# Optimization experiments

Hardware: AMD Instinct MI355X
Metric: run time of the kernel (lower is better)

The kernel has to match this reference:

```python
import jax, jax.numpy as jnp
import numpy as np

DIM = 96
HEADS = 4
HID = int(DIM * 2.66)  # 255, GDFN hidden width
B, H, W = 4, 128, 128


def _conv(x, w, b=None, groups=1):
    y = jax.lax.conv_general_dilated(x, w, (1, 1), 'SAME',
                                     dimension_numbers=('NCHW', 'OIHW', 'NCHW'),
                                     feature_group_count=groups)
    return y if b is None else y + b[None, :, None, None]


def _ln(x, w, b):
    # WithBias LayerNorm over channel dim (per pixel), biased variance, eps=1e-5
    mu = x.mean(1, keepdims=True)
    var = ((x - mu) ** 2).mean(1, keepdims=True)
    return (x - mu) / jnp.sqrt(var + 1e-5) * w[None, :, None, None] + b[None, :, None, None]


def _l2norm(x):
    # torch F.normalize(dim=-1): x / max(||x||_2, 1e-12)
    return x / jnp.maximum(jnp.linalg.norm(x, axis=-1, keepdims=True), 1e-12)


def _gelu(x):
    return jax.nn.gelu(x, approximate=False)


def setup_inputs() -> dict:
    key = jax.random.key(0)
    ks = iter(jax.random.split(key, 32))
    nrm = lambda shp, s=0.02: jax.random.normal(next(ks), shp, dtype=jnp.float32) * s
    d, h2 = DIM, HID
    inp = {
        'x': jax.random.normal(next(ks), (B, DIM, H, W), dtype=jnp.float32),
        # L_conv: 3x3(d->d,+b) GELU 1x1(d->1,+b)
        'Lc_w1': nrm((d, d, 3, 3)), 'Lc_b1': jnp.zeros((d,), jnp.float32),
        'Lc_w2': nrm((1, d, 1, 1)), 'Lc_b2': jnp.zeros((1,), jnp.float32),
        # R_conv: 3x3(d->d,+b) GELU 1x1(d->3,+b)
        'Rc_w1': nrm((d, d, 3, 3)), 'Rc_b1': jnp.zeros((d,), jnp.float32),
        'Rc_w2': nrm((3, d, 1, 1)), 'Rc_b2': jnp.zeros((3,), jnp.float32),
        # L_rein: 3x3(1->d,+b) GELU ; R_rein: 3x3(3->d,+b)
        'Lr_w': nrm((d, 1, 3, 3)), 'Lr_b': jnp.zeros((d,), jnp.float32),
        'Rr_w': nrm((d, 3, 3, 3)), 'Rr_b': jnp.zeros((d,), jnp.float32),
        # LayerNorms (WithBias)
        'n1_w': jnp.ones((d,), jnp.float32), 'n1_b': jnp.zeros((d,), jnp.float32),
        'nL_w': jnp.ones((d,), jnp.float32), 'nL_b': jnp.zeros((d,), jnp.float32),
        'n2_w': jnp.ones((d,), jnp.float32), 'n2_b': jnp.zeros((d,), jnp.float32),
        # Illum_Attention (bias=False)
        'temp': jnp.ones((HEADS, 1, 1), jnp.float32),
        'q_w': nrm((d, d, 1, 1)),
        'qd_w': nrm((d, d, 3, 3)),          # q_dwconv is a FULL 3x3 conv (no groups)
        'kv_w': nrm((2 * d, d, 1, 1)),
        'kvd_w': nrm((2 * d, 1, 3, 3)),     # depthwise, groups=2*dim
        'po_w': nrm((d, d, 1, 1)),
        # FeedForward (bias=False); NOTE: 'dwconv' here is a FULL 3x3 conv
        'pi_w': nrm((h2, d, 1, 1)),
        'fdw_w': nrm((h2, h2, 3, 3)),
        'fpo_w': nrm((d, h2, 1, 1)),
    }
    return inp


def reference(x, Lc_w1, Lc_b1, Lc_w2, Lc_b2, Rc_w1, Rc_b1, Rc_w2, Rc_b2,
              Lr_w, Lr_b, Rr_w, Rr_b, n1_w, n1_b, nL_w, nL_b, n2_w, n2_b,
              temp, q_w, qd_w, kv_w, kvd_w, po_w, pi_w, fdw_w, fpo_w):
    b, c, h, w = x.shape
    # Retinex decomposition heads
    L = _conv(_gelu(_conv(x, Lc_w1, Lc_b1)), Lc_w2, Lc_b2)   # [b,1,h,w]
    R = _conv(_gelu(_conv(x, Rc_w1, Rc_b1)), Rc_w2, Rc_b2)   # [b,3,h,w]
    L_rein = _gelu(_conv(jax.lax.stop_gradient(L), Lr_w, Lr_b))  # detach in torch
    R_rein = _conv(jax.lax.stop_gradient(R), Rr_w, Rr_b)
    # Illum_Guided_TransformerBlock: x = x + attn(norm1(x), normL(illum))
    xn = _ln(x, n1_w, n1_b)
    ill = _ln(L_rein, nL_w, nL_b)
    q = _conv(_conv(ill, q_w), qd_w)
    kv = _conv(_conv(xn, kv_w), kvd_w, groups=2 * c)
    k, v = jnp.split(kv, 2, axis=1)
    ch, hw = c // HEADS, h * w
    heads = lambda t: t.reshape(b, HEADS, ch, hw)
    qh, kh, vh = _l2norm(heads(q)), _l2norm(heads(k)), heads(v)
    # channel-wise attention: [b,heads,ch,ch]
    attn = jax.nn.softmax(jnp.einsum('bhci,bhdi->bhcd', qh, kh) * temp[None], axis=-1)
    out = jnp.einsum('bhcd,bhdi->bhci', attn, vh).reshape(b, c, h, w)
    x = x + _conv(out, po_w)
    # x = x + ffn(norm2(x))
    x2 = _ln(x, n2_w, n2_b)
    x = x + _conv(_gelu(_conv(_conv(x2, pi_w), fdw_w)), fpo_w)
    x = x + R_rein
    return (x, L, R)
```

## Files before the change

kernel.cpp:

```cpp
#include <hip/hip_runtime.h>

#define HWsz 16384
#define Wd 128

typedef unsigned short ushortT;
typedef unsigned int uintT;
typedef __attribute__((ext_vector_type(8))) short short8v;
typedef __attribute__((ext_vector_type(4))) float f32x4;
typedef __attribute__((ext_vector_type(16))) float f32x16;
typedef __attribute__((ext_vector_type(4))) unsigned short ushort4v;

__device__ __forceinline__ float gelu_f(float x){
    return 0.5f * x * (1.0f + erff(x * 0.70710678118654752f));
}
__device__ __forceinline__ ushortT f2b(float f){
    union { float f; uintT u; } v; v.f = f;
    uintT r = v.u + 0x7FFFu + ((v.u >> 16) & 1u);
    return (ushortT)(r >> 16);
}
__device__ __forceinline__ float b2f(ushortT u){
    union { uintT u; float f; } v; v.u = ((uintT)u) << 16; return v.f;
}
__device__ __forceinline__ void gload_lds16(const ushortT* g, ushortT* l){
    __builtin_amdgcn_global_load_lds(
        (const __attribute__((address_space(1))) void*)g,
        (__attribute__((address_space(3))) void*)l, 16, 0, 0);
}

__device__ __forceinline__ void pack3_one(int e, const float* __restrict__ w,
    ushortT* __restrict__ outp, int cout, int cin, int BN, int NCH)
{
    int j = e & 7; int r = e >> 3;
    int ocl = r % BN; r /= BN;
    int kg  = r & 3;  r >>= 2;
    int tap = r % 9;  r /= 9;
    int ch  = r % NCH;
    int nt  = r / NCH;
    int ci = ch*32 + kg*8 + j;
    int oc = nt*BN + ocl;
    float v = (oc < cout && ci < cin) ? w[((size_t)oc*cin + ci)*9 + tap] : 0.f;
    outp[e] = f2b(v);
}
__device__ __forceinline__ void pack1_one(int e, const float* __restrict__ w,
    ushortT* __restrict__ outp, int cout, int cin, int BN, int NCH)
{
    int j = e & 7; int r = e >> 3;
    int ocl = r % BN; r /= BN;
    int kg  = r & 3;  r >>= 2;
    int ch  = r % NCH;
    int nt  = r / NCH;
    int ci = ch*32 + kg*8 + j;
    int oc = nt*BN + ocl;
    float v = (oc < cout && ci < cin) ? w[(size_t)oc*cin + ci] : 0.f;
    outp[e] = f2b(v);
}
__global__ __launch_bounds__(256) void pack_all_kernel(
    const float* Lc, const float* Rc, const float* Qd, const float* Fd,
    const float* Q1, const float* KV1, const float* PI1, const float* FPO1,
    ushortT* dL, ushortT* dR, ushortT* dQ, ushortT* dF,
    ushortT* dq0, ushortT* dkv, ushortT* dpi, ushortT* dfpo)
{
    int e = blockIdx.x*256 + threadIdx.x;
    if      (e < 82944)  pack3_one(e,        Lc, dL, 96, 96, 48, 3);
    else if (e < 165888) pack3_one(e-82944,  Rc, dR, 96, 96, 48, 3);
    else if (e < 248832) pack3_one(e-165888, Qd, dQ, 96, 96, 32, 3);
    else if (e < 838656) pack3_one(e-248832, Fd, dF, 255,255, 64, 8);
    else if (e < 847872) pack1_one(e-838656, Q1, dq0, 96, 96, 96, 3);
    else if (e < 866304) pack1_one(e-847872, KV1,dkv, 192,96, 48, 3);
    else if (e < 890880) pack1_one(e-866304, PI1,dpi, 255,96, 64, 3);
    else if (e < 915456) pack1_one(e-890880, FPO1,dfpo,96,255, 96, 8);
}

__global__ __launch_bounds__(256) void tonhwc_kernel(
    const float* __restrict__ in, ushortT* __restrict__ outp)
{
    const int p = blockIdx.x*256 + threadIdx.x;
    const int b = blockIdx.y;
    const float* ip = in + (size_t)b*96*HWsz + p;
    ushortT* op = outp + ((size_t)b*HWsz + p)*96;
#pragma unroll
    for (int g=0; g<12; g++){
        float v[8];
#pragma unroll
        for (int c=0;c<8;c++) v[c] = ip[(size_t)(g*8+c)*HWsz];
        uint4 pk;
        pk.x = (uintT)f2b(v[0]) | ((uintT)f2b(v[1])<<16);
        pk.y = (uintT)f2b(v[2]) | ((uintT)f2b(v[3])<<16);
        pk.z = (uintT)f2b(v[4]) | ((uintT)f2b(v[5])<<16);
        pk.w = (uintT)f2b(v[6]) | ((uintT)f2b(v[7])<<16);
        *(uint4*)(op + g*8) = pk;
    }
}

template<int NG, int NCH, int ACT, int TWOOUT>
__global__ __launch_bounds__(256,2) void conv3x3_v4(
    const ushortT* __restrict__ inh,
    const ushortT* __restrict__ wpk1, const ushortT* __restrict__ wpk2,
    const float* __restrict__ bias1, const float* __restrict__ bias2,
    ushortT* __restrict__ out1, ushortT* __restrict__ out2,
    int cout, int ocpad)
{
    constexpr int BN = NG*16;
    constexpr int Cpad = NCH*32;
    constexpr int WCH4 = 9*4*BN;
    constexpr int WI = (WCH4 + 255)/256;
    __shared__ __align__(16) ushortT As[4*324*8];
    __shared__ __align__(16) ushortT Ws[WCH4*8];

    const int tid = threadIdx.x;
    const int l   = tid & 63;
    const int wv  = tid >> 6;
    const int l15 = l & 15;
    const int kg  = l >> 4;
    const int tix = blockIdx.x & 7, tiy = blockIdx.x >> 3;
    const int b   = blockIdx.z;
    const int x0 = tix*16, y0 = tiy*16;

    int nt = blockIdx.y;
    const ushortT* wpk; const float* bias; ushortT* outp; int ntw;
    if (TWOOUT && nt >= 2){ wpk = wpk2; bias = bias2; outp = out2; ntw = nt-2; }
    else { wpk = wpk1; bias = bias1; outp = out1; ntw = nt; }
    const int ocbase = ntw*BN;

    f32x4 acc[4][NG];
#pragma unroll
    for (int m=0;m<4;m++)
#pragma unroll
        for (int n=0;n<NG;n++) acc[m][n] = (f32x4){0.f,0.f,0.f,0.f};

    const ushortT* inb = inh + (size_t)b*HWsz*Cpad;

    for (int ch=0; ch<NCH; ch++){
        __syncthreads();
        for (int t=tid; t<1296; t+=256){
            int p = t>>2, g = t&3;
            int hy = p/18, hx = p - hy*18;
            int gy = y0 + hy - 1, gx = x0 + hx - 1;
            uint4 v; v.x=0u; v.y=0u; v.z=0u; v.w=0u;
            if ((unsigned)gy < 128u && (unsigned)gx < 128u)
                v = *(const uint4*)(inb + (size_t)(gy*Wd+gx)*Cpad + ch*32 + g*8);
            *(uint4*)(As + (g*324+p)*8) = v;
        }
        {
            const ushortT* wsrc = wpk + ((size_t)ntw*NCH + ch)*(WCH4*8);
#pragma unroll
            for (int i=0; i<WI; i++){
                int t = i*256 + tid;
                if ((WCH4 & 255) == 0 || t < WCH4)
                    gload_lds16(wsrc + (size_t)t*8, Ws + (size_t)t*8);
            }
        }
        __syncthreads();
#pragma unroll
        for (int tp=0; tp<9; tp++){
            const int dy = tp/3, dx = tp - dy*3;
            short8v bf[NG];
#pragma unroll
            for (int n=0;n<NG;n++)
                bf[n] = *(const short8v*)(Ws + ((size_t)(tp*4 + kg)*BN + n*16 + l15)*8);
#pragma unroll
            for (int mg=0;mg<4;mg++){
                short8v a = *(const short8v*)(As + (kg*324 + (wv*4+mg+dy)*18 + l15+dx)*8);
#pragma unroll
                for (int n=0;n<NG;n++)
                    acc[mg][n] = __builtin_amdgcn_mfma_f32_16x16x32_bf16(a, bf[n], acc[mg][n], 0,0,0);
            }
        }
    }
    __syncthreads();
    ushortT* Ts = As + wv*1024;
#pragma unroll
    for (int mg=0;mg<4;mg++){
        int gy = y0 + wv*4 + mg;
        ushortT* orow = outp + ((size_t)b*HWsz + gy*Wd + x0)*ocpad + ocbase;
#pragma unroll
        for (int n=0;n<NG;n++){
            int ocl = n*16 + l15;
            int oc  = ocbase + ocl;
            float bs = (bias && oc < cout) ? bias[oc] : 0.f;
#pragma unroll
            for (int j=0;j<4;j++){
                int pxj = kg*4 + j;
                float r = 0.f;
                if (oc < cout){ r = acc[mg][n][j] + bs; if (ACT) r = gelu_f(r); }
                int seg = ((ocl>>3) + pxj) & 7;
                Ts[pxj*64 + seg*8 + (ocl&7)] = f2b(r);
            }
        }
#pragma unroll
        for (int ps=0; ps < (BN+31)/32; ps++){
            int rpx = l & 15;
            int rs  = (l>>4) + ps*4;
            if (rs*8 < BN){
                int pseg = (rs + rpx) & 7;
                short8v v = *(const short8v*)(Ts + rpx*64 + pseg*8);
                *(short8v*)(orow + (size_t)rpx*ocpad + rs*8) = v;
            }
        }
    }
}

template<int NGW, int NCH>
__global__ __launch_bounds__(256) void gemm1x1_v2(
    const ushortT* __restrict__ inh, const ushortT* __restrict__ wpk,
    ushortT* __restrict__ outp, int cout, int ocpad)
{
    constexpr int BN = NGW*16;
    constexpr int Cpad = NCH*32;
    __shared__ __align__(16) ushortT Ts[4*16*64];

    const int tid = threadIdx.x;
    const int l = tid & 63, wv = tid >> 6, l15 = l & 15, kg = l >> 4;
    const int p0 = blockIdx.x*64;
    const int b  = blockIdx.z;
    const int nt = wv, ocbase = wv*BN;
    const ushortT* inb = inh + (size_t)b*HWsz*Cpad;

    f32x4 acc[4][NGW];
#pragma unroll
    for (int m=0;m<4;m++)
#pragma unroll
        for (int n=0;n<NGW;n++) acc[m][n] = (f32x4){0.f,0.f,0.f,0.f};

#pragma unroll
    for (int ch=0; ch<NCH; ch++){
        short8v a[4], bw[NGW];
#pragma unroll
        for (int mg=0; mg<4; mg++)
            a[mg] = *(const short8v*)(inb + (size_t)(p0 + mg*16 + l15)*Cpad + ch*32 + kg*8);
#pragma unroll
        for (int n=0;n<NGW;n++)
            bw[n] = *(const short8v*)(wpk + (((size_t)(nt*NCH + ch)*4 + kg)*BN + n*16 + l15)*8);
#pragma unroll
        for (int mg=0;mg<4;mg++)
#pragma unroll
            for (int n=0;n<NGW;n++)
                acc[mg][n] = __builtin_amdgcn_mfma_f32_16x16x32_bf16(a[mg], bw[n], acc[mg][n], 0,0,0);
    }
    ushortT* Tw = Ts + wv*1024;
#pragma unroll
    for (int mg=0;mg<4;mg++){
        ushortT* orow = outp + ((size_t)b*HWsz + p0 + mg*16)*ocpad + ocbase;
#pragma unroll
        for (int n=0;n<NGW;n++){
            int ocl = n*16 + l15;
            int oc  = ocbase + ocl;
#pragma unroll
            for (int j=0;j<4;j++){
                int pxj = kg*4 + j;
                float r = (oc < cout) ? acc[mg][n][j] : 0.f;
                int seg = ((ocl>>3) + pxj) & 7;
                Tw[pxj*64 + seg*8 + (ocl&7)] = f2b(r);
            }
        }
#pragma unroll
        for (int ps=0; ps < (BN+31)/32; ps++){
            int rpx = l & 15;
            int rs  = (l>>4) + ps*4;
            if (rs*8 < BN){
                int pseg = (rs + rpx) & 7;
                short8v v = *(const short8v*)(Tw + rpx*64 + pseg*8);
                *(short8v*)(orow + (size_t)rpx*ocpad + rs*8) = v;
            }
        }
    }
}

template<int NG, int NCH, int ACT, int OMODE, int NSPLIT, int XMAP>
__global__ __launch_bounds__(256,4) void conv3x3_mfma(
    const ushortT* __restrict__ inh,
    const ushortT* __restrict__ wpk1, const ushortT* __restrict__ wpk2,
    const float* __restrict__ bias1, const float* __restrict__ bias2,
    void* __restrict__ out1, void* __restrict__ out2,
    int cout, int ocpad)
{
    constexpr int BN = NG*16;
    constexpr int Cpad = NCH*32;
    __shared__ __align__(16) ushortT As[4*324*8];

    const int tid = threadIdx.x;
    const int l   = tid & 63;
    const int wv  = tid >> 6;
    const int l15 = l & 15;
    const int kg  = l >> 4;
    int tile = blockIdx.x, nt = blockIdx.y, b = blockIdx.z;
    const int tix = tile & 7, tiy = tile >> 3;

    const ushortT* wpk = wpk1; const float* bias = bias1; void* outv = out1;
    if (NSPLIT > 0 && nt >= NSPLIT){ nt -= NSPLIT; wpk = wpk2; bias = bias2; outv = out2; }

    f32x4 acc[4][NG];
#pragma unroll
    for (int m=0;m<4;m++)
#pragma unroll
        for (int n=0;n<NG;n++) acc[m][n] = (f32x4){0.f,0.f,0.f,0.f};

    const ushortT* inb = inh + (size_t)b*HWsz*Cpad;

    for (int ch=0; ch<NCH; ch++){
        __syncthreads();
#pragma unroll
        for (int g=0; g<4; g++){
            for (int p=tid; p<324; p+=256){
                int hy = p/18, hx = p - hy*18;
                int gy = tiy*16 + hy - 1, gx = tix*16 + hx - 1;
                uint4 v; v.x=0u; v.y=0u; v.z=0u; v.w=0u;
                if ((unsigned)gy < 128u && (unsigned)gx < 128u)
                    v = *(const uint4*)(inb + (size_t)(gy*Wd+gx)*Cpad + ch*32 + g*8);
                *(uint4*)(As + (g*324+p)*8) = v;
            }
        }
        __syncthreads();
        const ushortT* wch = wpk + (size_t)(nt*NCH + ch)*(9*4*BN*8);
#pragma unroll
        for (int tp=0; tp<9; tp++){
            const int dy = tp/3, dx = tp - dy*3;
            short8v a[4], bf[NG];
#pragma unroll
            for (int mg=0; mg<4; mg++){
                int p = (wv*4 + mg + dy)*18 + l15 + dx;
                a[mg] = *(const short8v*)(As + (kg*324 + p)*8);
            }
#pragma unroll
            for (int n=0;n<NG;n++)
                bf[n] = *(const short8v*)(wch + ((size_t)(tp*4 + kg)*BN + n*16 + l15)*8);
#pragma unroll
            for (int mg=0;mg<4;mg++)
#pragma unroll
                for (int n=0;n<NG;n++)
                    acc[mg][n] = __builtin_amdgcn_mfma_f32_16x16x32_bf16(a[mg], bf[n], acc[mg][n], 0,0,0);
        }
    }
    if (OMODE == 2){
        ushortT* out = (ushortT*)outv;
#pragma unroll
        for (int n=0;n<NG;n++){
            int oc = nt*BN + n*16 + l15;
            if (oc < cout){
                float bs = bias ? bias[oc] : 0.f;
#pragma unroll
                for (int mg=0;mg<4;mg++){
                    int gy = tiy*16 + wv*4 + mg;
                    int gx = tix*16 + kg*4;
                    ushort4v pk;
#pragma unroll
                    for (int j=0;j<4;j++){
                        float r = acc[mg][n][j] + bs;
                        if (ACT) r = gelu_f(r);
                        pk[j] = f2b(r);
                    }
                    *(ushort4v*)(out + ((size_t)b*cout + oc)*HWsz + gy*Wd + gx) = pk;
                }
            }
        }
    }
}

template<int NG, int NCH, int RES, int OMODE, int XMAP>
__global__ __launch_bounds__(256) void gemm1x1_mfma(
    const ushortT* __restrict__ inh, const ushortT* __restrict__ wpk, int wstride_z,
    const float* __restrict__ res1, const ushortT* __restrict__ res2b,
    void* __restrict__ outv, int cout, int ocpad)
{
    constexpr int BN = NG*16;
    constexpr int Cpad = NCH*32;
    constexpr int LSTR = (BN <= 64) ? 64 : 128;
    constexpr int MASK = LSTR/8 - 1;
    __shared__ __align__(16) ushortT TsS[(OMODE==1) ? 4*16*LSTR : 16];

    const int tid = threadIdx.x;
    const int l = tid & 63, wv = tid >> 6, l15 = l & 15, kg = l >> 4;
    int chunk = blockIdx.x, nt = blockIdx.y, b = blockIdx.z;
    const int p0 = chunk*256 + wv*64;
    const ushortT* inb = inh + (size_t)b*HWsz*Cpad;
    const ushortT* wp  = wpk + (size_t)b*wstride_z;

    f32x4 acc[4][NG];
#pragma unroll
    for (int m=0;m<4;m++)
#pragma unroll
        for (int n=0;n<NG;n++) acc[m][n] = (f32x4){0.f,0.f,0.f,0.f};

#pragma unroll
    for (int ch=0; ch<NCH; ch++){
        short8v a[4], bw[NG];
#pragma unroll
        for (int mg=0; mg<4; mg++)
            a[mg] = *(const short8v*)(inb + (size_t)(p0 + mg*16 + l15)*Cpad + ch*32 + kg*8);
#pragma unroll
        for (int n=0;n<NG;n++)
            bw[n] = *(const short8v*)(wp + (((size_t)(nt*NCH + ch)*4 + kg)*BN + n*16 + l15)*8);
#pragma unroll
        for (int mg=0;mg<4;mg++)
#pragma unroll
            for (int n=0;n<NG;n++)
                acc[mg][n] = __builtin_amdgcn_mfma_f32_16x16x32_bf16(a[mg], bw[n], acc[mg][n], 0,0,0);
    }
    if (OMODE == 0){
        float* out = (float*)outv;
#pragma unroll
        for (int n=0;n<NG;n++){
            int oc = nt*BN + n*16 + l15;
            if (oc < cout){
#pragma unroll
                for (int mg=0;mg<4;mg++){
                    int pix = p0 + mg*16 + kg*4;
                    size_t idx = ((size_t)b*cout + oc)*HWsz + pix;
                    float4 r;
                    r.x = acc[mg][n][0]; r.y = acc[mg][n][1];
                    r.z = acc[mg][n][2]; r.w = acc[mg][n][3];
                    if (RES>=1){ float4 q = *(const float4*)(res1+idx); r.x+=q.x;r.y+=q.y;r.z+=q.z;r.w+=q.w; }
                    if (RES>=2){
                        ushort4v q = *(const ushort4v*)(res2b+idx);
                        r.x+=b2f(q[0]); r.y+=b2f(q[1]); r.z+=b2f(q[2]); r.w+=b2f(q[3]);
                    }
                    *(float4*)(out + idx) = r;
                }
            }
        }
    } else {
        ushortT* outp = (ushortT*)outv;
        ushortT* Ts = TsS + wv*(16*LSTR);
#pragma unroll
        for (int mg=0;mg<4;mg++){
            ushortT* orow = outp + ((size_t)b*HWsz + p0 + mg*16)*ocpad + nt*BN;
#pragma unroll
            for (int n=0;n<NG;n++){
                int ocl = n*16 + l15;
                int oc  = nt*BN + ocl;
#pragma unroll
                for (int j=0;j<4;j++){
                    int pxj = kg*4 + j;
                    float r = (oc < cout) ? acc[mg][n][j] : 0.f;
                    int seg = ((ocl>>3) + pxj) & MASK;
                    Ts[pxj*LSTR + seg*8 + (ocl&7)] = f2b(r);
                }
            }
#pragma unroll
            for (int ps=0; ps < (BN+31)/32; ps++){
                int rpx = l & 15;
                int rs  = (l>>4) + ps*4;
                if (rs*8 < BN){
                    int pseg = (rs + rpx) & MASK;
                    short8v v = *(const short8v*)(Ts + rpx*LSTR + pseg*8);
                    *(short8v*)(orow + (size_t)rpx*ocpad + rs*8) = v;
                }
            }
        }
    }
}

template<int NOUT>
__global__ __launch_bounds__(256) void head1x1_kernel(
    const ushortT* __restrict__ inh, const float* __restrict__ w,
    const float* __restrict__ bias, float* __restrict__ out)
{
    __shared__ float lw[NOUT*96];
    const int tid = threadIdx.x;
    for (int t=tid; t<NOUT*96; t+=256) lw[t] = w[t];
    __syncthreads();
    const int p = blockIdx.x*256 + tid;
    const int b = blockIdx.y;
    const ushortT* ip = inh + ((size_t)b*HWsz + p)*96;
    float v[96];
#pragma unroll
    for (int g=0; g<12; g++){
        short8v s = *(const short8v*)(ip + g*8);
#pragma unroll
        for (int i=0;i<8;i++) v[g*8+i] = b2f((ushortT)s[i]);
    }
#pragma unroll
    for (int oc=0; oc<NOUT; oc++){
        float acc = bias[oc];
#pragma unroll
        for (int c=0;c<96;c++) acc += v[c]*lw[oc*96+c];
        out[((size_t)b*NOUT + oc)*HWsz + p] = acc;
    }
}

__global__ __launch_bounds__(256) void lrein_ln_kernel(
    const float* __restrict__ L, const float* __restrict__ w,
    const float* __restrict__ bias, const float* __restrict__ lnw,
    const float* __restrict__ lnb, ushortT* __restrict__ outh)
{
    __shared__ float sw[864], sb[96], sn1[96], sn2[96];
    const int tid = threadIdx.x;
    for (int t=tid; t<864; t+=256) sw[t] = w[t];
    if (tid < 96){ sb[tid]=bias[tid]; sn1[tid]=lnw[tid]; sn2[tid]=lnb[tid]; }
    __syncthreads();
    const int p = blockIdx.x*256 + tid;
    const int b = blockIdx.y;
    const int y = p>>7, x = p&127;
    const float* ib = L + (size_t)b*HWsz;
    float win[9];
#pragma unroll
    for (int dy=0;dy<3;dy++)
#pragma unroll
        for (int dx=0;dx<3;dx++){
            int gy=y+dy-1, gx=x+dx-1;
            win[dy*3+dx] = ((unsigned)gy<128u && (unsigned)gx<128u) ? ib[gy*Wd+gx] : 0.f;
        }
    float v[96]; float s=0.f;
#pragma unroll
    for (int c=0;c<96;c++){
        float a = sb[c];
#pragma unroll
        for (int t=0;t<9;t++) a += win[t]*sw[c*9+t];
        a = gelu_f(a);
        v[c]=a; s+=a;
    }
    const float mu = s*(1.f/96.f);
    float s2=0.f;
#pragma unroll
    for (int c=0;c<96;c++){ float d=v[c]-mu; s2+=d*d; }
    const float inv = 1.f/sqrtf(s2*(1.f/96.f)+1e-5f);
    ushortT* op = outh + ((size_t)b*HWsz + p)*96;
#pragma unroll
    for (int g=0; g<12; g++){
        uint4 pk; uintT w4[4];
#pragma unroll
        for (int i=0;i<4;i++){
            float r0 = (v[g*8+2*i]-mu)*inv*sn1[g*8+2*i]+sn2[g*8+2*i];
            float r1 = (v[g*8+2*i+1]-mu)*inv*sn1[g*8+2*i+1]+sn2[g*8+2*i+1];
            w4[i] = (uintT)f2b(r0) | ((uintT)f2b(r1)<<16);
        }
        pk.x=w4[0]; pk.y=w4[1]; pk.z=w4[2]; pk.w=w4[3];
        *(uint4*)(op + g*8) = pk;
    }
}

__global__ __launch_bounds__(256) void ln_n2n_kernel(
    const float* __restrict__ in, const float* __restrict__ w,
    const float* __restrict__ bias, ushortT* __restrict__ outh)
{
    const int p = blockIdx.x*256+threadIdx.x;
    const int b = blockIdx.y;
    const float* ip = in + (size_t)b*96*HWsz + p;
    float v[96]; float s=0.f;
#pragma unroll
    for(int c=0;c<96;c++){ v[c]=ip[(size_t)c*HWsz]; s+=v[c]; }
    const float mu = s*(1.f/96.f);
    float s2=0.f;
#pragma unroll
    for(int c=0;c<96;c++){ float d=v[c]-mu; s2+=d*d; }
    const float inv = 1.f/sqrtf(s2*(1.f/96.f)+1e-5f);
    ushortT* op = outh + ((size_t)b*HWsz + p)*96;
#pragma unroll
    for (int g=0; g<12; g++){
        uint4 pk; uintT w4[4];
#pragma unroll
        for (int i=0;i<4;i++){
            float r0 = (v[g*8+2*i]-mu)*inv*w[g*8+2*i]+bias[g*8+2*i];
            float r1 = (v[g*8+2*i+1]-mu)*inv*w[g*8+2*i+1]+bias[g*8+2*i+1];
            w4[i] = (uintT)f2b(r0) | ((uintT)f2b(r1)<<16);
        }
        pk.x=w4[0]; pk.y=w4[1]; pk.z=w4[2]; pk.w=w4[3];
        *(uint4*)(op + g*8) = pk;
    }
}

__global__ __launch_bounds__(256) void conv3x3_rr_kernel(
    const float* __restrict__ in, const float* __restrict__ w,
    const float* __restrict__ bias, ushortT* __restrict__ out)
{
    __shared__ float sw[216], sb[8];
    const int oc0 = blockIdx.y*8;
    if (threadIdx.x < 216) sw[threadIdx.x] = w[(size_t)oc0*27 + threadIdx.x];
    if (threadIdx.x < 8)   sb[threadIdx.x] = bias[oc0 + threadIdx.x];
    __syncthreads();
    const int p = blockIdx.x*256+threadIdx.x;
    const int b = blockIdx.z;
    const int y=p>>7, x=p&127;
    const float* ib = in + (size_t)b*3*HWsz;
    float win[27];
#pragma unroll
    for (int ci=0;ci<3;ci++)
#pragma unroll
        for (int dy=0;dy<3;dy++)
#pragma unroll
            for (int dx=0;dx<3;dx++){
                int gy=y+dy-1, gx=x+dx-1;
                win[ci*9+dy*3+dx] = ((unsigned)gy<128u && (unsigned)gx<128u)
                    ? ib[(size_t)ci*HWsz + gy*Wd+gx] : 0.f;
            }
#pragma unroll
    for (int i=0;i<8;i++){
        float acc = sb[i];
#pragma unroll
        for (int t=0;t<27;t++) acc += win[t]*sw[i*27+t];
        out[((size_t)b*96 + oc0+i)*HWsz + p] = f2b(acc);
    }
}

__global__ __launch_bounds__(256) void dw_nhwc_kernel(
    const ushortT* __restrict__ inh, const float* __restrict__ w,
    ushortT* __restrict__ kout, ushortT* __restrict__ vouth)
{
    const int p = blockIdx.x*256+threadIdx.x;
    const int c0 = blockIdx.y*8;
    const int b = blockIdx.z;
    const int y=p>>7, x=p&127;
    float lw[72];
#pragma unroll
    for (int i=0;i<8;i++)
#pragma unroll
        for (int t=0;t<9;t++) lw[i*9+t] = w[(size_t)(c0+i)*9 + t];
    const ushortT* ib = inh + (size_t)b*HWsz*192;
    float acc[8];
#pragma unroll
    for (int i=0;i<8;i++) acc[i]=0.f;
#pragma unroll
    for(int dy=0;dy<3;dy++){
        int gy=y+dy-1;
        if((unsigned)gy<128u){
#pragma unroll
            for(int dx=0;dx<3;dx++){
                int gx=x+dx-1;
                if((unsigned)gx<128u){
                    short8v s = *(const short8v*)(ib + (size_t)(gy*Wd+gx)*192 + c0);
#pragma unroll
                    for (int i=0;i<8;i++) acc[i] += b2f((ushortT)s[i])*lw[i*9+dy*3+dx];
                }
            }
        }
    }
    if (c0 < 96){
#pragma unroll
        for (int i=0;i<8;i++)
            kout[((size_t)b*96 + c0+i)*HWsz + p] = f2b(acc[i]);
    } else {
        ushortT* op = vouth + ((size_t)b*HWsz + p)*96 + (c0-96);
        uint4 pk;
        pk.x = (uintT)f2b(acc[0]) | ((uintT)f2b(acc[1])<<16);
        pk.y = (uintT)f2b(acc[2]) | ((uintT)f2b(acc[3])<<16);
        pk.z = (uintT)f2b(acc[4]) | ((uintT)f2b(acc[5])<<16);
        pk.w = (uintT)f2b(acc[6]) | ((uintT)f2b(acc[7])<<16);
        *(uint4*)op = pk;
    }
}

__global__ __launch_bounds__(256) void rownorm_bf16_kernel(
    const ushortT* __restrict__ qb, const ushortT* __restrict__ kb,
    float* __restrict__ invqk)
{
    __shared__ float red[256];
    const int r = blockIdx.x;
    const ushortT* ip = (r < 384) ? (qb + (size_t)r*HWsz) : (kb + (size_t)(r-384)*HWsz);
    float s=0.f;
    const ushortT* tp = ip + threadIdx.x*64;
#pragma unroll
    for (int g=0; g<8; g++){
        short8v v = *(const short8v*)(tp + g*8);
#pragma unroll
        for (int i=0;i<8;i++){ float f = b2f((ushortT)v[i]); s += f*f; }
    }
    red[threadIdx.x]=s; __syncthreads();
    for(int st=128; st>0; st>>=1){
        if(threadIdx.x<st) red[threadIdx.x]+=red[threadIdx.x+st];
        __syncthreads();
    }
    if(threadIdx.x==0) invqk[r] = 1.f/fmaxf(sqrtf(red[0]), 1e-12f);
}

__global__ __launch_bounds__(256) void qk_mfma_kernel(
    const ushortT* __restrict__ qb, const ushortT* __restrict__ kb,
    float* __restrict__ part)
{
    const int tid = threadIdx.x;
    const int l = tid & 63, wv = tid >> 6;
    const int chunk = blockIdx.x*4 + wv;
    const int bh = blockIdx.y, b = bh>>2, h = bh&3;
    const int ch = min(l & 31, 23);
    const int kh = (l >> 5)*8;
    const ushortT* qp = qb + ((size_t)b*96 + h*24 + ch)*HWsz + chunk*512 + kh;
    const ushortT* kp = kb + ((size_t)b*96 + h*24 + ch)*HWsz + chunk*512 + kh;
    f32x16 acc;
#pragma unroll
    for (int r=0;r<16;r++) acc[r]=0.f;
    for (int ks=0; ks<32; ks++){
        short8v a  = *(const short8v*)(qp + ks*16);
        short8v bb = *(const short8v*)(kp + ks*16);
        acc = __builtin_amdgcn_mfma_f32_32x32x16_bf16(a, bb, acc, 0,0,0);
    }
    float* op = part + ((size_t)chunk*16 + bh)*1024;
    const int col = l & 31;
#pragma unroll
    for (int r=0;r<16;r++){
        int row = (r&3) + 8*(r>>2) + 4*(l>>5);
        op[row*32 + col] = acc[r];
    }
}

__global__ void qk_reduce_kernel(const float* __restrict__ part, float* __restrict__ out)
{
    int idx = blockIdx.x*256+threadIdx.x;
    float s=0.f;
    for(int c=0;c<32;c++) s += part[(size_t)c*16384 + idx];
    out[idx]=s;
}

__global__ __launch_bounds__(576) void softmax_kernel(
    const float* __restrict__ raw, const float* __restrict__ invq,
    const float* __restrict__ invk, const float* __restrict__ temp,
    float* __restrict__ attn)
{
    __shared__ float l[576];
    const int bh=blockIdx.x, b=bh>>2, h=bh&3;
    const int tid=threadIdx.x;
    const int i=tid/24, j=tid-i*24;
    l[tid] = raw[(size_t)bh*1024 + i*32 + j] * invq[b*96+h*24+i] * invk[b*96+h*24+j] * temp[h];
    __syncthreads();
    if(tid<24){
        float m=-1e30f;
#pragma unroll
        for(int jj=0;jj<24;jj++) m = fmaxf(m, l[tid*24+jj]);
        float e[24]; float s=0.f;
#pragma unroll
        for(int jj=0;jj<24;jj++){ e[jj]=__expf(l[tid*24+jj]-m); s+=e[jj]; }
        float isv = 1.f/s;
#pragma unroll
        for(int jj=0;jj<24;jj++) attn[(size_t)bh*576 + tid*24 + jj] = e[jj]*isv;
    }
}

__global__ __launch_bounds__(256) void mkM_kernel(
    const float* __restrict__ attn, const float* __restrict__ po_w,
    ushortT* __restrict__ Mpk)
{
    const int b = blockIdx.x;
    for (int e = threadIdx.x; e < 9216; e += 256){
        int oc = e / 96, d = e - oc*96;
        int h = d / 24, dl = d - h*24;
        const float* aw = attn + ((size_t)(b*4+h))*576 + dl;
        const float* pw = po_w + (size_t)oc*96 + h*24;
        float s = 0.f;
#pragma unroll
        for (int c=0;c<24;c++) s += pw[c]*aw[c*24];
        int ch = d>>5, kg = (d>>3)&3, j = d&7;
        Mpk[(size_t)b*9216 + ((size_t)(ch*4+kg)*96 + oc)*8 + j] = f2b(s);
    }
}

extern "C" void kernel_launch(void* const* d_in, const int* in_sizes, int n_in,
                              void* d_out, int out_size, void* d_ws, size_t ws_size,
                              hipStream_t stream)
{
    const float* x     = (const float*)d_in[0];
    const float* Lc_w1 = (const float*)d_in[1];
    const float* Lc_b1 = (const float*)d_in[2];
    const float* Lc_w2 = (const float*)d_in[3];
    const float* Lc_b2 = (const float*)d_in[4];
    const float* Rc_w1 = (const float*)d_in[5];
    const float* Rc_b1 = (const float*)d_in[6];
    const float* Rc_w2 = (const float*)d_in[7];
    const float* Rc_b2 = (const float*)d_in[8];
    const float* Lr_w  = (const float*)d_in[9];
    const float* Lr_b  = (const float*)d_in[10];
    const float* Rr_w  = (const float*)d_in[11];
    const float* Rr_b  = (const float*)d_in[12];
    const float* n1_w  = (const float*)d_in[13];
    const float* n1_b  = (const float*)d_in[14];
    const float* nL_w  = (const float*)d_in[15];
    const float* nL_b  = (const float*)d_in[16];
    const float* n2_w  = (const float*)d_in[17];
    const float* n2_b  = (const float*)d_in[18];
    const float* temp  = (const float*)d_in[19];
    const float* q_w   = (const float*)d_in[20];
    const float* qd_w  = (const float*)d_in[21];
    const float* kv_w  = (const float*)d_in[22];
    const float* kvd_w = (const float*)d_in[23];
    const float* po_w  = (const float*)d_in[24];
    const float* pi_w  = (const float*)d_in[25];
    const float* fdw_w = (const float*)d_in[26];
    const float* fpo_w = (const float*)d_in[27];

    char* base = (char*)d_ws;
    ushortT* xh   = (ushortT*)(base + 0);
    ushortT* f0h  = (ushortT*)(base + 0);
    ushortT* Lh   = (ushortT*)(base + 33554432);
    ushortT* kv0h = (ushortT*)(base + 33554432);
    ushortT* f1h  = (ushortT*)(base + 33554432);
    ushortT* Rh   = (ushortT*)(base + 67108864);
    ushortT* vh   = (ushortT*)(base + 67108864);
    ushortT* x2nh = (ushortT*)(base + 67108864);
    ushortT* illh = (ushortT*)(base + 79691776);
    ushortT* xnh  = (ushortT*)(base + 92274688);
    ushortT* q0h  = (ushortT*)(base + 104857600);
    ushortT* qb   = (ushortT*)(base + 117440512);
    float*   x1   = (float*)(base + 117440512);
    ushortT* kb   = (ushortT*)(base + 142606336);
    ushortT* Bb   = (ushortT*)(base + 155189248);
    char* smb = base + 167772160;
    ushortT* wpkL = (ushortT*)smb;   smb += 165888;
    ushortT* wpkR = (ushortT*)smb;   smb += 165888;
    ushortT* wpkQ = (ushortT*)smb;   smb += 165888;
    ushortT* wpkF = (ushortT*)smb;   smb += 1179648;
    ushortT* wq0  = (ushortT*)smb;   smb += 18432;
    ushortT* wkv  = (ushortT*)smb;   smb += 36864;
    ushortT* wpi  = (ushortT*)smb;   smb += 49152;
    ushortT* wfpo = (ushortT*)smb;   smb += 49152;
    ushortT* Mpk  = (ushortT*)smb;   smb += 73728;
    float* invqk  = (float*)smb;     smb += 3072;
    float* part   = (float*)smb;     smb += 2097152;
    float* araw   = (float*)smb;     smb += 65536;
    float* attn   = (float*)smb;     smb += 36864;

    float* out_x = (float*)d_out;
    float* out_L = out_x + (size_t)4*96*HWsz;
    float* out_R = out_L + (size_t)4*HWsz;

    dim3 blk(256);

    hipLaunchKernelGGL(pack_all_kernel, dim3(3576), blk, 0, stream,
        Lc_w1, Rc_w1, qd_w, fdw_w, q_w, kv_w, pi_w, fpo_w,
        wpkL, wpkR, wpkQ, wpkF, wq0, wkv, wpi, wfpo);
    hipLaunchKernelGGL(tonhwc_kernel, dim3(64,4), blk, 0, stream, x, xh);

    hipLaunchKernelGGL((conv3x3_v4<3,3,1,1>), dim3(64,4,4), blk, 0, stream,
        xh, wpkL, wpkR, Lc_b1, Rc_b1, Lh, Rh, 96, 96);
    hipLaunchKernelGGL((head1x1_kernel<1>), dim3(64,4), blk, 0, stream, Lh, Lc_w2, Lc_b2, out_L);
    hipLaunchKernelGGL((head1x1_kernel<3>), dim3(64,4), blk, 0, stream, Rh, Rc_w2, Rc_b2, out_R);
    hipLaunchKernelGGL(lrein_ln_kernel, dim3(64,4), blk, 0, stream, out_L, Lr_w, Lr_b, nL_w, nL_b, illh);
    hipLaunchKernelGGL(conv3x3_rr_kernel, dim3(64,12,4), blk, 0, stream, out_R, Rr_w, Rr_b, Bb);

    hipLaunchKernelGGL(ln_n2n_kernel, dim3(64,4), blk, 0, stream, x, n1_w, n1_b, xnh);

    hipLaunchKernelGGL((gemm1x1_mfma<6,3,0,1,0>), dim3(64,1,4), blk, 0, stream,
        illh, wq0, 0, nullptr, nullptr, (void*)q0h, 96, 96);
    hipLaunchKernelGGL((conv3x3_mfma<2,3,0,2,0,0>), dim3(64,3,4), blk, 0, stream,
        q0h, wpkQ, wpkQ, nullptr, nullptr, (void*)qb, (void*)qb, 96, 0);
    hipLaunchKernelGGL((gemm1x1_v2<3,3>), dim3(256,1,4), blk, 0, stream,
        xnh, wkv, kv0h, 192, 192);
    hipLaunchKernelGGL(dw_nhwc_kernel, dim3(64,24,4), blk, 0, stream, kv0h, kvd_w, kb, vh);

    hipLaunchKernelGGL(rownorm_bf16_kernel, dim3(768), blk, 0, stream, qb, kb, invqk);
    hipLaunchKernelGGL(qk_mfma_kernel, dim3(8,16), blk, 0, stream, qb, kb, part);
    hipLaunchKernelGGL(qk_reduce_kernel, dim3(64), blk, 0, stream, part, araw);
    hipLaunchKernelGGL(softmax_kernel, dim3(16), dim3(576), 0, stream, araw, invqk, invqk+384, temp, attn);
    hipLaunchKernelGGL(mkM_kernel, dim3(4), blk, 0, stream, attn, po_w, Mpk);
    hipLaunchKernelGGL((gemm1x1_mfma<6,3,1,0,0>), dim3(64,1,4), blk, 0, stream,
        vh, Mpk, 9216, x, nullptr, (void*)x1, 96, 0);

    hipLaunchKernelGGL(ln_n2n_kernel, dim3(64,4), blk, 0, stream, x1, n2_w, n2_b, x2nh);
    hipLaunchKernelGGL((gemm1x1_v2<4,3>), dim3(256,1,4), blk, 0, stream,
        x2nh, wpi, f0h, 255, 256);
    hipLaunchKernelGGL((conv3x3_v4<4,8,1,0>), dim3(64,4,4), blk, 0, stream,
        f0h, wpkF, wpkF, nullptr, nullptr, f1h, f1h, 255, 256);
    hipLaunchKernelGGL((gemm1x1_mfma<6,8,2,0,0>), dim3(64,1,4), blk, 0, stream,
        f1h, wfpo, 0, x1, Bb, (void*)out_x, 96, 0);
}
```

Before: 376.9 us.

## Fuse LayerNorms into NHWC conversion and attention-projection GEMM; retile FFN conv

The first LayerNorm now runs inside the NCHW-to-NHWC conversion kernel, so x is read once and both the bf16 copy and the normalized copy are written in the same pass. A new kernel fuses the attention-output GEMM, the residual add and the second LayerNorm, using a cross-lane shuffle reduction for the per-pixel statistics. This removes two standalone LayerNorm passes over the full activation. The FFN 3x3 conv is retiled from 64-wide to 48-wide output groups with more blocks, its weight packing is updated to match, and conv3x3_v4 launch bounds are raised to allow 3 blocks per SM. The fused LayerNorm computes variance as E[x^2]-mu^2, which is slightly less numerically robust.

```diff
diff --git a/kernel.cpp b/kernel.cpp
--- a/kernel.cpp
+++ b/kernel.cpp
@@ -64,36 +64,51 @@
     if      (e < 82944)  pack3_one(e,        Lc, dL, 96, 96, 48, 3);
     else if (e < 165888) pack3_one(e-82944,  Rc, dR, 96, 96, 48, 3);
     else if (e < 248832) pack3_one(e-165888, Qd, dQ, 96, 96, 32, 3);
-    else if (e < 838656) pack3_one(e-248832, Fd, dF, 255,255, 64, 8);
-    else if (e < 847872) pack1_one(e-838656, Q1, dq0, 96, 96, 96, 3);
-    else if (e < 866304) pack1_one(e-847872, KV1,dkv, 192,96, 48, 3);
-    else if (e < 890880) pack1_one(e-866304, PI1,dpi, 255,96, 64, 3);
-    else if (e < 915456) pack1_one(e-890880, FPO1,dfpo,96,255, 96, 8);
-}
-
-__global__ __launch_bounds__(256) void tonhwc_kernel(
-    const float* __restrict__ in, ushortT* __restrict__ outp)
+    else if (e < 912384) pack3_one(e-248832, Fd, dF, 255,255, 48, 8);
+    else if (e < 921600) pack1_one(e-912384, Q1, dq0, 96, 96, 96, 3);
+    else if (e < 940032) pack1_one(e-921600, KV1,dkv, 192,96, 48, 3);
+    else if (e < 964608) pack1_one(e-940032, PI1,dpi, 255,96, 64, 3);
+    else if (e < 989184) pack1_one(e-964608, FPO1,dfpo,96,255, 96, 8);
+}
+
+__global__ __launch_bounds__(256) void tonhwc_ln_kernel(
+    const float* __restrict__ in, const float* __restrict__ w,
+    const float* __restrict__ bias, ushortT* __restrict__ xh,
+    ushortT* __restrict__ xnh)
 {
     const int p = blockIdx.x*256 + threadIdx.x;
     const int b = blockIdx.y;
     const float* ip = in + (size_t)b*96*HWsz + p;
-    ushortT* op = outp + ((size_t)b*HWsz + p)*96;
+    float v[96]; float s=0.f;
+#pragma unroll
+    for(int c=0;c<96;c++){ v[c]=ip[(size_t)c*HWsz]; s+=v[c]; }
+    const float mu = s*(1.f/96.f);
+    float s2=0.f;
+#pragma unroll
+    for(int c=0;c<96;c++){ float d=v[c]-mu; s2+=d*d; }
+    const float inv = 1.f/sqrtf(s2*(1.f/96.f)+1e-5f);
+    ushortT* op1 = xh  + ((size_t)b*HWsz + p)*96;
+    ushortT* op2 = xnh + ((size_t)b*HWsz + p)*96;
 #pragma unroll
     for (int g=0; g<12; g++){
-        float v[8];
-#pragma unroll
-        for (int c=0;c<8;c++) v[c] = ip[(size_t)(g*8+c)*HWsz];
-        uint4 pk;
-        pk.x = (uintT)f2b(v[0]) | ((uintT)f2b(v[1])<<16);
-        pk.y = (uintT)f2b(v[2]) | ((uintT)f2b(v[3])<<16);
-        pk.z = (uintT)f2b(v[4]) | ((uintT)f2b(v[5])<<16);
-        pk.w = (uintT)f2b(v[6]) | ((uintT)f2b(v[7])<<16);
-        *(uint4*)(op + g*8) = pk;
+        uint4 pk1, pk2; uintT a4[4], n4[4];
+#pragma unroll
+        for (int i=0;i<4;i++){
+            float x0 = v[g*8+2*i], x1v = v[g*8+2*i+1];
+            a4[i] = (uintT)f2b(x0) | ((uintT)f2b(x1v)<<16);
+            float r0 = (x0-mu)*inv*w[g*8+2*i]+bias[g*8+2*i];
+            float r1 = (x1v-mu)*inv*w[g*8+2*i+1]+bias[g*8+2*i+1];
+            n4[i] = (uintT)f2b(r0) | ((uintT)f2b(r1)<<16);
+        }
+        pk1.x=a4[0]; pk1.y=a4[1]; pk1.z=a4[2]; pk1.w=a4[3];
+        pk2.x=n4[0]; pk2.y=n4[1]; pk2.z=n4[2]; pk2.w=n4[3];
+        *(uint4*)(op1 + g*8) = pk1;
+        *(uint4*)(op2 + g*8) = pk2;
     }
 }
 
 template<int NG, int NCH, int ACT, int TWOOUT>
-__global__ __launch_bounds__(256,2) void conv3x3_v4(
+__global__ __launch_bounds__(256,3) void conv3x3_v4(
     const ushortT* __restrict__ inh,
     const ushortT* __restrict__ wpk1, const ushortT* __restrict__ wpk2,
     const float* __restrict__ bias1, const float* __restrict__ bias2,
@@ -450,6 +465,108 @@
     }
 }
 
+__global__ __launch_bounds__(256) void pvpo_ln_kernel(
+    const ushortT* __restrict__ vh, const ushortT* __restrict__ Mpk,
+    const float* __restrict__ xres, const float* __restrict__ lnw,
+    const float* __restrict__ lnb, float* __restrict__ x1out,
+    ushortT* __restrict__ x2nh)
+{
+    constexpr int BN = 96, NG = 6, NCH = 3, Cpad = 96, LSTR = 128, MASK = 15;
+    __shared__ __align__(16) ushortT TsS[4*16*LSTR];
+
+    const int tid = threadIdx.x;
+    const int l = tid & 63, wv = tid >> 6, l15 = l & 15, kg = l >> 4;
+    const int b = blockIdx.z;
+    const int p0 = blockIdx.x*256 + wv*64;
+    const ushortT* inb = vh + (size_t)b*HWsz*Cpad;
+    const ushortT* wp  = Mpk + (size_t)b*9216;
+
+    f32x4 acc[4][NG];
+#pragma unroll
+    for (int m=0;m<4;m++)
+#pragma unroll
+        for (int n=0;n<NG;n++) acc[m][n] = (f32x4){0.f,0.f,0.f,0.f};
+
+#pragma unroll
+    for (int ch=0; ch<NCH; ch++){
+        short8v a[4], bw[NG];
+#pragma unroll
+        for (int mg=0; mg<4; mg++)
+            a[mg] = *(const short8v*)(inb + (size_t)(p0 + mg*16 + l15)*Cpad + ch*32 + kg*8);
+#pragma unroll
+        for (int n=0;n<NG;n++)
+            bw[n] = *(const short8v*)(wp + (((size_t)ch*4 + kg)*BN + n*16 + l15)*8);
+#pragma unroll
+        for (int mg=0;mg<4;mg++)
+#pragma unroll
+            for (int n=0;n<NG;n++)
+                acc[mg][n] = __builtin_amdgcn_mfma_f32_16x16x32_bf16(a[mg], bw[n], acc[mg][n], 0,0,0);
+    }
+    float mu_[4], inv_[4];
+#pragma unroll
+    for (int mg=0;mg<4;mg++){
+#pragma unroll
+        for (int n=0;n<NG;n++){
+            int oc = n*16 + l15;
+            int pix = p0 + mg*16 + kg*4;
+            size_t idx = ((size_t)b*96 + oc)*HWsz + pix;
+            float4 q = *(const float4*)(xres+idx);
+            acc[mg][n][0] += q.x; acc[mg][n][1] += q.y;
+            acc[mg][n][2] += q.z; acc[mg][n][3] += q.w;
+            float4 r;
+            r.x = acc[mg][n][0]; r.y = acc[mg][n][1];
+            r.z = acc[mg][n][2]; r.w = acc[mg][n][3];
+            *(float4*)(x1out + idx) = r;
+        }
+    }
+    float nv[4][NG][4];
+#pragma unroll
+    for (int mg=0;mg<4;mg++){
+#pragma unroll
+        for (int j=0;j<4;j++){
+            float s = 0.f, s2 = 0.f;
+#pragma unroll
+            for (int n=0;n<NG;n++){ float v = acc[mg][n][j]; s += v; s2 += v*v; }
+#pragma unroll
+            for (int m=1; m<16; m<<=1){
+                s  += __shfl_xor(s, m, 64);
+                s2 += __shfl_xor(s2, m, 64);
+            }
+            float mu = s*(1.f/96.f);
+            float var = s2*(1.f/96.f) - mu*mu;
+            float inv = 1.f/sqrtf(var + 1e-5f);
+#pragma unroll
+            for (int n=0;n<NG;n++){
+                int oc = n*16 + l15;
+                nv[mg][n][j] = (acc[mg][n][j]-mu)*inv*lnw[oc]+lnb[oc];
+            }
+        }
+    }
+    ushortT* Ts = TsS + wv*(16*LSTR);
+#pragma unroll
+    for (int mg=0;mg<4;mg++){
+        ushortT* orow = x2nh + ((size_t)b*HWsz + p0 + mg*16)*96;
+#pragma unroll
+        for (int n=0;n<NG;n++){
+            int ocl = n*16 + l15;
+#pragma unroll
+            for (int j=0;j<4;j++){
+                int pxj = kg*4 + j;
+                int seg = ((ocl>>3) + pxj) & MASK;
+                Ts[pxj*LSTR + seg*8 + (ocl&7)] = f2b(nv[mg][n][j]);
+            }
+        }
+#pragma unroll
+        for (int ps=0; ps<3; ps++){
+            int rpx = l & 15;
+            int rs  = (l>>4) + ps*4;
+            int pseg = (rs + rpx) & MASK;
+            short8v v = *(const short8v*)(Ts + rpx*LSTR + pseg*8);
+            *(short8v*)(orow + (size_t)rpx*96 + rs*8) = v;
+        }
+    }
+}
+
 template<int NOUT>
 __global__ __launch_bounds__(256) void head1x1_kernel(
     const ushortT* __restrict__ inh, const float* __restrict__ w,
@@ -522,36 +639,6 @@
         for (int i=0;i<4;i++){
             float r0 = (v[g*8+2*i]-mu)*inv*sn1[g*8+2*i]+sn2[g*8+2*i];
             float r1 = (v[g*8+2*i+1]-mu)*inv*sn1[g*8+2*i+1]+sn2[g*8+2*i+1];
-            w4[i] = (uintT)f2b(r0) | ((uintT)f2b(r1)<<16);
-        }
-        pk.x=w4[0]; pk.y=w4[1]; pk.z=w4[2]; pk.w=w4[3];
-        *(uint4*)(op + g*8) = pk;
-    }
-}
-
-__global__ __launch_bounds__(256) void ln_n2n_kernel(
-    const float* __restrict__ in, const float* __restrict__ w,
-    const float* __restrict__ bias, ushortT* __restrict__ outh)
-{
-    const int p = blockIdx.x*256+threadIdx.x;
-    const int b = blockIdx.y;
-    const float* ip = in + (size_t)b*96*HWsz + p;
-    float v[96]; float s=0.f;
-#pragma unroll
-    for(int c=0;c<96;c++){ v[c]=ip[(size_t)c*HWsz]; s+=v[c]; }
-    const float mu = s*(1.f/96.f);
-    float s2=0.f;
-#pragma unroll
-    for(int c=0;c<96;c++){ float d=v[c]-mu; s2+=d*d; }
-    const float inv = 1.f/sqrtf(s2*(1.f/96.f)+1e-5f);
-    ushortT* op = outh + ((size_t)b*HWsz + p)*96;
-#pragma unroll
-    for (int g=0; g<12; g++){
-        uint4 pk; uintT w4[4];
-#pragma unroll
-        for (int i=0;i<4;i++){
-            float r0 = (v[g*8+2*i]-mu)*inv*w[g*8+2*i]+bias[g*8+2*i];
-            float r1 = (v[g*8+2*i+1]-mu)*inv*w[g*8+2*i+1]+bias[g*8+2*i+1];
             w4[i] = (uintT)f2b(r0) | ((uintT)f2b(r1)<<16);
         }
         pk.x=w4[0]; pk.y=w4[1]; pk.z=w4[2]; pk.w=w4[3];
@@ -794,7 +881,7 @@
     ushortT* wpkL = (ushortT*)smb;   smb += 165888;
     ushortT* wpkR = (ushortT*)smb;   smb += 165888;
     ushortT* wpkQ = (ushortT*)smb;   smb += 165888;
-    ushortT* wpkF = (ushortT*)smb;   smb += 1179648;
+    ushortT* wpkF = (ushortT*)smb;   smb += 1327104;
     ushortT* wq0  = (ushortT*)smb;   smb += 18432;
     ushortT* wkv  = (ushortT*)smb;   smb += 36864;
     ushortT* wpi  = (ushortT*)smb;   smb += 49152;
@@ -811,10 +898,10 @@
 
     dim3 blk(256);
 
-    hipLaunchKernelGGL(pack_all_kernel, dim3(3576), blk, 0, stream,
+    hipLaunchKernelGGL(pack_all_kernel, dim3(3864), blk, 0, stream,
         Lc_w1, Rc_w1, qd_w, fdw_w, q_w, kv_w, pi_w, fpo_w,
         wpkL, wpkR, wpkQ, wpkF, wq0, wkv, wpi, wfpo);
-    hipLaunchKernelGGL(tonhwc_kernel, dim3(64,4), blk, 0, stream, x, xh);
+    hipLaunchKernelGGL(tonhwc_ln_kernel, dim3(64,4), blk, 0, stream, x, n1_w, n1_b, xh, xnh);
 
     hipLaunchKernelGGL((conv3x3_v4<3,3,1,1>), dim3(64,4,4), blk, 0, stream,
         xh, wpkL, wpkR, Lc_b1, Rc_b1, Lh, Rh, 96, 96);
@@ -822,8 +909,6 @@
     hipLaunchKernelGGL((head1x1_kernel<3>), dim3(64,4), blk, 0, stream, Rh, Rc_w2, Rc_b2, out_R);
     hipLaunchKernelGGL(lrein_ln_kernel, dim3(64,4), blk, 0, stream, out_L, Lr_w, Lr_b, nL_w, nL_b, illh);
     hipLaunchKernelGGL(conv3x3_rr_kernel, dim3(64,12,4), blk, 0, stream, out_R, Rr_w, Rr_b, Bb);
-
-    hipLaunchKernelGGL(ln_n2n_kernel, dim3(64,4), blk, 0, stream, x, n1_w, n1_b, xnh);
 
     hipLaunchKernelGGL((gemm1x1_mfma<6,3,0,1,0>), dim3(64,1,4), blk, 0, stream,
         illh, wq0, 0, nullptr, nullptr, (void*)q0h, 96, 96);
@@ -838,13 +923,12 @@
     hipLaunchKernelGGL(qk_reduce_kernel, dim3(64), blk, 0, stream, part, araw);
     hipLaunchKernelGGL(softmax_kernel, dim3(16), dim3(576), 0, stream, araw, invqk, invqk+384, temp, attn);
     hipLaunchKernelGGL(mkM_kernel, dim3(4), blk, 0, stream, attn, po_w, Mpk);
-    hipLaunchKernelGGL((gemm1x1_mfma<6,3,1,0,0>), dim3(64,1,4), blk, 0, stream,
-        vh, Mpk, 9216, x, nullptr, (void*)x1, 96, 0);
-
-    hipLaunchKernelGGL(ln_n2n_kernel, dim3(64,4), blk, 0, stream, x1, n2_w, n2_b, x2nh);
+    hipLaunchKernelGGL(pvpo_ln_kernel, dim3(64,1,4), blk, 0, stream,
+        vh, Mpk, x, n2_w, n2_b, x1, x2nh);
+
     hipLaunchKernelGGL((gemm1x1_v2<4,3>), dim3(256,1,4), blk, 0, stream,
         x2nh, wpi, f0h, 255, 256);
-    hipLaunchKernelGGL((conv3x3_v4<4,8,1,0>), dim3(64,4,4), blk, 0, stream,
+    hipLaunchKernelGGL((conv3x3_v4<3,8,1,0>), dim3(64,6,4), blk, 0, stream,
         f0h, wpkF, wpkF, nullptr, nullptr, f1h, f1h, 255, 256);
     hipLaunchKernelGGL((gemm1x1_mfma<6,8,2,0,0>), dim3(64,1,4), blk, 0, stream,
         f1h, wfpo, 0, x1, Bb, (void*)out_x, 96, 0);
```

Result: no change. 373.6 us (-0.9%).
